# Performance work log

Hardware: AMD Instinct MI355X
Metric: run time of the kernel (lower is better)

The kernel has to match this reference:

```python
import jax, jax.numpy as jnp
import numpy as np

B, IN, OUT = 4096, 1024, 1024
HALF_PI = np.pi / 2.0
TWO_PI = 2.0 * np.pi
# cyclic control-point index table per quadrant (from the torch module)
CPI = jnp.array([[3, 0, 1, 2], [0, 1, 2, 3], [1, 2, 3, 0], [2, 3, 0, 1]], dtype=jnp.int32)
# Catmull-Rom cubic spline basis (4 control points, [t^3,t^2,t,1] monomials)
BASIS = np.array([[-0.5, 1.5, -1.5, 0.5],
                  [1.0, -2.5, 2.0, -0.5],
                  [-0.5, 0.0, 0.5, 0.0],
                  [0.0, 1.0, 0.0, 0.0]], dtype=np.float32)


def setup_inputs() -> dict:
    key = jax.random.key(0)
    k_x, k_p, k_w, k_b = jax.random.split(key, 4)
    x = jax.random.normal(k_x, (B, IN), dtype=jnp.float32)
    phase = jax.random.uniform(k_p, (B,), dtype=jnp.float32) * TWO_PI
    # kaiming_uniform_(a=sqrt(5)) on each (OUT, IN) slice -> bound = 1/sqrt(fan_in)
    bound = 1.0 / np.sqrt(IN)
    weights = jax.random.uniform(k_w, (4, OUT, IN), dtype=jnp.float32, minval=-bound, maxval=bound)
    biases = jax.random.uniform(k_b, (4, OUT), dtype=jnp.float32, minval=-bound, maxval=bound)
    basis = jnp.asarray(BASIS)
    return {"input": x, "phase": phase, "weights": weights, "biases": biases, "basis": basis}


def reference(input, phase, weights, biases, basis):
    # quadrant index q in {0,1,2,3}; same selection as the nested torch.where chain
    q = jnp.clip(jnp.floor(phase / HALF_PI).astype(jnp.int32), 0, 3)          # (B,)
    t = phase / HALF_PI - q.astype(phase.dtype)                                # (B,), in [0,1)
    tt = jnp.stack([t ** 3, t ** 2, t, jnp.ones_like(t)], axis=-1)             # (B,4)
    coeffs = tt @ basis                                                        # (B,4) spline coeffs
    idx = CPI[q]                                                               # (B,4) control-point ids
    # Instead of materializing per-sample (B,OUT,IN) weights, contract input against
    # all 4 control-point matrices (same math: w_b = sum_k c_k W_{idx_k}).
    z = jnp.einsum('bi,coi->bco', input, weights)                              # (B,4,OUT)
    zg = jnp.take_along_axis(z, idx[:, :, None], axis=1)                       # (B,4,OUT)
    bg = biases[idx]                                                           # (B,4,OUT)
    return jnp.einsum('bk,bko->bo', coeffs, zg + bg)                           # (B,OUT)
```

## Files before the change

kernel.cpp:

```cpp
#include <hip/hip_runtime.h>
#include <stdint.h>

#define BATCH   4096
#define IN_DIM  1024
#define OUT_DIM 1024

typedef __bf16 bf16x8 __attribute__((ext_vector_type(8)));
typedef float  f32x4  __attribute__((ext_vector_type(4)));

__device__ __forceinline__ uint16_t f2bf(float f) {
    union { float f; uint32_t u; } v; v.f = f;
    uint32_t u = v.u;
    uint32_t r = (u + 0x7FFFu + ((u >> 16) & 1u)) >> 16;
    return (uint16_t)r;
}

__device__ __forceinline__ float bf2f(uint16_t h) {
    union { uint32_t u; float f; } v; v.u = ((uint32_t)h) << 16;
    return v.f;
}

__global__ __launch_bounds__(256) void prep(
    const float* __restrict__ x, const float* __restrict__ phase,
    const float* __restrict__ basis, const float* __restrict__ W,
    uint16_t* __restrict__ xb, uint16_t* __restrict__ Wb,
    float* __restrict__ alphaWS)
{
    const int bid = blockIdx.x;
    const int tid = threadIdx.x;

    if (bid < BATCH) {
        const int b = bid;
        const float HALF_PI = 1.5707963267948966f;
        float s  = phase[b] / HALF_PI;
        int   q  = (int)floorf(s);
        q = q < 0 ? 0 : (q > 3 ? 3 : q);
        float t  = s - (float)q;
        float t2 = t * t, t3 = t2 * t;

        float coef[4];
#pragma unroll
        for (int j = 0; j < 4; ++j)
            coef[j] = t3 * basis[j] + t2 * basis[4 + j] + t * basis[8 + j] + basis[12 + j];

        if (tid < 4) alphaWS[b * 4 + tid] = coef[(tid - q + 1) & 3];

        float4 xv = ((const float4*)(x + (size_t)b * IN_DIM))[tid];
        ushort4 o;
        o.x = f2bf(xv.x); o.y = f2bf(xv.y); o.z = f2bf(xv.z); o.w = f2bf(xv.w);
        ((ushort4*)(xb + (size_t)b * IN_DIM))[tid] = o;
    } else {
        const int j = bid - BATCH;
        float4 wv = ((const float4*)W)[j * 256 + tid];
        ushort4 o;
        o.x = f2bf(wv.x); o.y = f2bf(wv.y); o.z = f2bf(wv.z); o.w = f2bf(wv.w);
        ((ushort4*)Wb)[j * 256 + tid] = o;
    }
}

__global__ __launch_bounds__(256, 4) void gemm_split(
    const uint16_t* __restrict__ xb, const uint16_t* __restrict__ Wb,
    uint16_t* __restrict__ P)
{
    __shared__ uint16_t As[128 * 64];
    __shared__ uint16_t Bs[128 * 64];

    const int tid  = threadIdx.x;
    const int lane = tid & 63;
    const int wid  = tid >> 6;
    const int wm   = wid >> 1;
    const int wn   = wid & 1;
    const int tileM = blockIdx.x * 128;
    const int tileN = blockIdx.y * 128;
    const int c     = blockIdx.z;

    f32x4 acc[4][4];
#pragma unroll
    for (int mi = 0; mi < 4; ++mi)
#pragma unroll
        for (int ni = 0; ni < 4; ++ni)
            acc[mi][ni] = (f32x4){0.f, 0.f, 0.f, 0.f};

    const int srow = lane >> 3;
    const int gchunk = ((lane & 7) ^ srow) * 8;

    const uint16_t* Ag = xb + (size_t)tileM * 1024;
    const uint16_t* Bg = Wb + ((size_t)c << 20) + (size_t)tileN * 1024;

    const int quad = lane >> 4;
    const int l7   = lane & 7;

    for (int kt = 0; kt < 16; ++kt) {
        const int k0 = kt * 64;
#pragma unroll
        for (int j = 0; j < 4; ++j) {
            const int s = wid * 4 + j;
            const uint16_t* ga = Ag + (size_t)(s * 8 + srow) * 1024 + k0 + gchunk;
            __builtin_amdgcn_global_load_lds(
                (const __attribute__((address_space(1))) void*)ga,
                (__attribute__((address_space(3))) void*)(As + s * 512), 16, 0, 0);
            const uint16_t* gb = Bg + (size_t)(s * 8 + srow) * 1024 + k0 + gchunk;
            __builtin_amdgcn_global_load_lds(
                (const __attribute__((address_space(1))) void*)gb,
                (__attribute__((address_space(3))) void*)(Bs + s * 512), 16, 0, 0);
        }
        __syncthreads();

#pragma unroll
        for (int ks = 0; ks < 2; ++ks) {
            bf16x8 af[4], bfr[4];
#pragma unroll
            for (int mi = 0; mi < 4; ++mi) {
                const int row = wm * 64 + mi * 16 + (lane & 15);
                const int ch  = (ks * 4 + quad) ^ l7;
                af[mi] = *(const bf16x8*)(As + row * 64 + ch * 8);
            }
#pragma unroll
            for (int ni = 0; ni < 4; ++ni) {
                const int row = wn * 64 + ni * 16 + (lane & 15);
                const int ch  = (ks * 4 + quad) ^ l7;
                bfr[ni] = *(const bf16x8*)(Bs + row * 64 + ch * 8);
            }
#pragma unroll
            for (int mi = 0; mi < 4; ++mi)
#pragma unroll
                for (int ni = 0; ni < 4; ++ni)
                    acc[mi][ni] = __builtin_amdgcn_mfma_f32_16x16x32_bf16(
                        af[mi], bfr[ni], acc[mi][ni], 0, 0, 0);
        }
        __syncthreads();
    }

    uint16_t* Pc = P + (size_t)c * (BATCH * (size_t)OUT_DIM);
    const int col0 = tileN + wn * 64 + (lane & 15);
#pragma unroll
    for (int mi = 0; mi < 4; ++mi) {
#pragma unroll
        for (int r = 0; r < 4; ++r) {
            const int m = tileM + wm * 64 + mi * 16 + quad * 4 + r;
#pragma unroll
            for (int ni = 0; ni < 4; ++ni)
                Pc[(size_t)m * OUT_DIM + col0 + ni * 16] = f2bf(acc[mi][ni][r]);
        }
    }
}

__global__ __launch_bounds__(256) void reduce_k(
    const uint16_t* __restrict__ P, const float* __restrict__ alphaWS,
    const float* __restrict__ biases, float* __restrict__ out)
{
    const int m = blockIdx.x;
    const int t = threadIdx.x;
    const size_t stride = (size_t)BATCH * OUT_DIM;

    const float4 al = *(const float4*)(alphaWS + 4 * m);
    float4 r = {0.f, 0.f, 0.f, 0.f};
    const float a[4] = {al.x, al.y, al.z, al.w};
#pragma unroll
    for (int c = 0; c < 4; ++c) {
        ushort4 p = ((const ushort4*)(P + c * stride + (size_t)m * OUT_DIM))[t];
        float4 b  = ((const float4*)(biases + c * OUT_DIM))[t];
        r.x += a[c] * (bf2f(p.x) + b.x);
        r.y += a[c] * (bf2f(p.y) + b.y);
        r.z += a[c] * (bf2f(p.z) + b.z);
        r.w += a[c] * (bf2f(p.w) + b.w);
    }
    ((float4*)(out + (size_t)m * OUT_DIM))[t] = r;
}

extern "C" void kernel_launch(void* const* d_in, const int* in_sizes, int n_in,
                              void* d_out, int out_size, void* d_ws, size_t ws_size,
                              hipStream_t stream)
{
    const float* x       = (const float*)d_in[0];
    const float* phase   = (const float*)d_in[1];
    const float* weights = (const float*)d_in[2];
    const float* biases  = (const float*)d_in[3];
    const float* basis   = (const float*)d_in[4];
    float* out = (float*)d_out;

    uint16_t* xb = (uint16_t*)d_ws;
    uint16_t* Wb = xb + (size_t)BATCH * IN_DIM;
    float* alphaWS = (float*)(Wb + (size_t)4 * OUT_DIM * IN_DIM);
    uint16_t* P = (uint16_t*)(alphaWS + (size_t)BATCH * 4);

    prep<<<2 * BATCH, 256, 0, stream>>>(x, phase, basis, weights, xb, Wb, alphaWS);

    dim3 grid(BATCH / 128, OUT_DIM / 128, 4);
    gemm_split<<<grid, 256, 0, stream>>>(xb, Wb, P);

    reduce_k<<<BATCH, 256, 0, stream>>>(P, alphaWS, biases, out);
}
```

Before: 131.1 us.

## Fuse control-point reduction into GEMM with per-wave control-point split

Replaces the split GEMM that writes four bf16 partial matrices, plus the separate reduction kernel, with one fused kernel. Each block computes a 64x64 output tile and assigns one control-point weight matrix to each wave. The waves share the A tile and reduce their alpha-scaled partials through LDS before adding biases and writing fp32 output. This removes the large intermediate P write/read and one launch. In exchange the tiles are smaller (less reuse of A per block) and occupancy drops to 3 blocks per SM.

```diff
diff --git a/kernel.cpp b/kernel.cpp
--- a/kernel.cpp
+++ b/kernel.cpp
@@ -58,21 +58,23 @@
     }
 }
 
-__global__ __launch_bounds__(256, 4) void gemm_split(
+#define PS 66
+
+__global__ __launch_bounds__(256, 3) void gemm_fused(
     const uint16_t* __restrict__ xb, const uint16_t* __restrict__ Wb,
-    uint16_t* __restrict__ P)
+    const float* __restrict__ alphaWS, const float* __restrict__ biases,
+    float* __restrict__ out)
 {
-    __shared__ uint16_t As[128 * 64];
-    __shared__ uint16_t Bs[128 * 64];
+    __shared__ uint16_t lds[64 * 64 + 4 * 64 * 64];
+    uint16_t* As = lds;
+    uint16_t* Bs = lds + 4096;
+    uint16_t* Ps = lds;
 
     const int tid  = threadIdx.x;
     const int lane = tid & 63;
     const int wid  = tid >> 6;
-    const int wm   = wid >> 1;
-    const int wn   = wid & 1;
-    const int tileM = blockIdx.x * 128;
-    const int tileN = blockIdx.y * 128;
-    const int c     = blockIdx.z;
+    const int tileM = blockIdx.x * 64;
+    const int tileN = blockIdx.y * 64;
 
     f32x4 acc[4][4];
 #pragma unroll
@@ -85,7 +87,7 @@
     const int gchunk = ((lane & 7) ^ srow) * 8;
 
     const uint16_t* Ag = xb + (size_t)tileM * 1024;
-    const uint16_t* Bg = Wb + ((size_t)c << 20) + (size_t)tileN * 1024;
+    const uint16_t* Bg = Wb + ((size_t)wid << 20) + (size_t)tileN * 1024;
 
     const int quad = lane >> 4;
     const int l7   = lane & 7;
@@ -93,33 +95,35 @@
     for (int kt = 0; kt < 16; ++kt) {
         const int k0 = kt * 64;
 #pragma unroll
-        for (int j = 0; j < 4; ++j) {
-            const int s = wid * 4 + j;
+        for (int j = 0; j < 2; ++j) {
+            const int s = wid * 2 + j;
             const uint16_t* ga = Ag + (size_t)(s * 8 + srow) * 1024 + k0 + gchunk;
             __builtin_amdgcn_global_load_lds(
                 (const __attribute__((address_space(1))) void*)ga,
                 (__attribute__((address_space(3))) void*)(As + s * 512), 16, 0, 0);
-            const uint16_t* gb = Bg + (size_t)(s * 8 + srow) * 1024 + k0 + gchunk;
+        }
+#pragma unroll
+        for (int j = 0; j < 8; ++j) {
+            const uint16_t* gb = Bg + (size_t)(j * 8 + srow) * 1024 + k0 + gchunk;
             __builtin_amdgcn_global_load_lds(
                 (const __attribute__((address_space(1))) void*)gb,
-                (__attribute__((address_space(3))) void*)(Bs + s * 512), 16, 0, 0);
+                (__attribute__((address_space(3))) void*)(Bs + wid * 4096 + j * 512), 16, 0, 0);
         }
         __syncthreads();
 
 #pragma unroll
         for (int ks = 0; ks < 2; ++ks) {
+            const int ch = (ks * 4 + quad) ^ l7;
             bf16x8 af[4], bfr[4];
 #pragma unroll
             for (int mi = 0; mi < 4; ++mi) {
-                const int row = wm * 64 + mi * 16 + (lane & 15);
-                const int ch  = (ks * 4 + quad) ^ l7;
+                const int row = mi * 16 + (lane & 15);
                 af[mi] = *(const bf16x8*)(As + row * 64 + ch * 8);
             }
 #pragma unroll
             for (int ni = 0; ni < 4; ++ni) {
-                const int row = wn * 64 + ni * 16 + (lane & 15);
-                const int ch  = (ks * 4 + quad) ^ l7;
-                bfr[ni] = *(const bf16x8*)(Bs + row * 64 + ch * 8);
+                const int row = ni * 16 + (lane & 15);
+                bfr[ni] = *(const bf16x8*)(Bs + wid * 4096 + row * 64 + ch * 8);
             }
 #pragma unroll
             for (int mi = 0; mi < 4; ++mi)
@@ -131,41 +135,63 @@
         __syncthreads();
     }
 
-    uint16_t* Pc = P + (size_t)c * (BATCH * (size_t)OUT_DIM);
-    const int col0 = tileN + wn * 64 + (lane & 15);
+    float av[4][4];
+#pragma unroll
+    for (int mi = 0; mi < 4; ++mi)
+#pragma unroll
+        for (int r = 0; r < 4; ++r)
+            av[mi][r] = alphaWS[(size_t)(tileM + mi * 16 + quad * 4 + r) * 4 + wid];
+
 #pragma unroll
     for (int mi = 0; mi < 4; ++mi) {
 #pragma unroll
         for (int r = 0; r < 4; ++r) {
-            const int m = tileM + wm * 64 + mi * 16 + quad * 4 + r;
+            const int row = mi * 16 + quad * 4 + r;
 #pragma unroll
             for (int ni = 0; ni < 4; ++ni)
-                Pc[(size_t)m * OUT_DIM + col0 + ni * 16] = f2bf(acc[mi][ni][r]);
-        }
-    }
-}
-
-__global__ __launch_bounds__(256) void reduce_k(
-    const uint16_t* __restrict__ P, const float* __restrict__ alphaWS,
-    const float* __restrict__ biases, float* __restrict__ out)
-{
-    const int m = blockIdx.x;
-    const int t = threadIdx.x;
-    const size_t stride = (size_t)BATCH * OUT_DIM;
-
-    const float4 al = *(const float4*)(alphaWS + 4 * m);
-    float4 r = {0.f, 0.f, 0.f, 0.f};
-    const float a[4] = {al.x, al.y, al.z, al.w};
-#pragma unroll
-    for (int c = 0; c < 4; ++c) {
-        ushort4 p = ((const ushort4*)(P + c * stride + (size_t)m * OUT_DIM))[t];
-        float4 b  = ((const float4*)(biases + c * OUT_DIM))[t];
-        r.x += a[c] * (bf2f(p.x) + b.x);
-        r.y += a[c] * (bf2f(p.y) + b.y);
-        r.z += a[c] * (bf2f(p.z) + b.z);
-        r.w += a[c] * (bf2f(p.w) + b.w);
-    }
-    ((float4*)(out + (size_t)m * OUT_DIM))[t] = r;
+                Ps[wid * (64 * PS) + row * PS + ni * 16 + (lane & 15)] =
+                    f2bf(av[mi][r] * acc[mi][ni][r]);
+        }
+    }
+    __syncthreads();
+
+    {
+        const int rr = tid >> 2;
+        const int cg = tid & 3;
+        const int colb = cg * 16;
+        const float4 al = *(const float4*)(alphaWS + (size_t)(tileM + rr) * 4);
+        const float a[4] = {al.x, al.y, al.z, al.w};
+
+        float res[16];
+#pragma unroll
+        for (int j = 0; j < 16; ++j) res[j] = 0.f;
+
+#pragma unroll
+        for (int cc = 0; cc < 4; ++cc) {
+#pragma unroll
+            for (int jj = 0; jj < 4; ++jj) {
+                float4 bv = *(const float4*)(biases + (size_t)cc * OUT_DIM + tileN + colb + jj * 4);
+                res[jj * 4 + 0] += a[cc] * bv.x;
+                res[jj * 4 + 1] += a[cc] * bv.y;
+                res[jj * 4 + 2] += a[cc] * bv.z;
+                res[jj * 4 + 3] += a[cc] * bv.w;
+            }
+            const uint16_t* p = Ps + cc * (64 * PS) + rr * PS + colb;
+#pragma unroll
+            for (int jj = 0; jj < 8; ++jj) {
+                uint32_t pv = *(const uint32_t*)(p + jj * 2);
+                res[jj * 2 + 0] += bf2f((uint16_t)(pv & 0xFFFFu));
+                res[jj * 2 + 1] += bf2f((uint16_t)(pv >> 16));
+            }
+        }
+
+        float* orow = out + (size_t)(tileM + rr) * OUT_DIM + tileN + colb;
+#pragma unroll
+        for (int jj = 0; jj < 4; ++jj) {
+            float4 o = {res[jj * 4 + 0], res[jj * 4 + 1], res[jj * 4 + 2], res[jj * 4 + 3]};
+            *(float4*)(orow + jj * 4) = o;
+        }
+    }
 }
 
 extern "C" void kernel_launch(void* const* d_in, const int* in_sizes, int n_in,
@@ -182,12 +208,9 @@
     uint16_t* xb = (uint16_t*)d_ws;
     uint16_t* Wb = xb + (size_t)BATCH * IN_DIM;
     float* alphaWS = (float*)(Wb + (size_t)4 * OUT_DIM * IN_DIM);
-    uint16_t* P = (uint16_t*)(alphaWS + (size_t)BATCH * 4);
 
     prep<<<2 * BATCH, 256, 0, stream>>>(x, phase, basis, weights, xb, Wb, alphaWS);
 
-    dim3 grid(BATCH / 128, OUT_DIM / 128, 4);
-    gemm_split<<<grid, 256, 0, stream>>>(xb, Wb, P);
-
-    reduce_k<<<BATCH, 256, 0, stream>>>(P, alphaWS, biases, out);
-}
+    dim3 grid(BATCH / 64, OUT_DIM / 64);
+    gemm_fused<<<grid, 256, 0, stream>>>(xb, Wb, alphaWS, biases, out);
+}
```

After: 130.0 us. Within noise of the previous version (-0.8%).
